# Kernel tuning notes

Measured on AMD Instinct MI355X. Metric: run time of the kernel, lower is better.

Reference implementation:

```python
import jax, jax.numpy as jnp
import numpy as np

U, I, D, B, E = 100000, 50000, 128, 4, 500000


def setup_inputs() -> dict:
    key = jax.random.key(0)
    ks = jax.random.split(key, 8)
    return {
        "init_user_embedding": jax.random.normal(ks[0], (U, D), dtype=jnp.float32),
        "init_item_embedding": jax.random.normal(ks[1], (I, D), dtype=jnp.float32),
        "edge_u": jax.random.randint(ks[2], (B, E), 0, U, dtype=jnp.int32),
        "edge_i": jax.random.randint(ks[3], (B, E), 0, I, dtype=jnp.int32),
        "edge_w": jax.random.uniform(ks[4], (B, E), dtype=jnp.float32),
        "u_w": jax.random.normal(ks[5], (D, D), dtype=jnp.float32) * (6.0 / (D + D)) ** 0.5,
        "i_w": jax.random.normal(ks[6], (D, D), dtype=jnp.float32) * (6.0 / (D + D)) ** 0.5,
        "alpha": jnp.full((1,), 0.25, dtype=jnp.float32),  # PReLU weight (default init 0.25)
    }


def reference(init_user_embedding, init_item_embedding, edge_u, edge_i, edge_w, u_w, i_w, alpha):
    # spmm per behavior: behavior_mats[b] @ item_emb and behavior_mats_t[b] @ user_emb
    def spmm_u(w, iu, ii):  # [U, D] = A[b] @ item_emb
        return jax.ops.segment_sum(w[:, None] * init_item_embedding[ii], iu, num_segments=U)

    def spmm_i(w, iu, ii):  # [I, D] = A[b].T @ user_emb
        return jax.ops.segment_sum(w[:, None] * init_user_embedding[iu], ii, num_segments=I)

    user_embs = jax.vmap(spmm_u)(edge_w, edge_u, edge_i)  # [B, U, D]
    item_embs = jax.vmap(spmm_i)(edge_w, edge_u, edge_i)  # [B, I, D]

    prelu = lambda x: jnp.where(x >= 0, x, alpha * x)

    multi_u = prelu(jnp.mean(user_embs, axis=0) @ u_w)    # [U, D]
    multi_i = prelu(jnp.mean(item_embs, axis=0) @ i_w)    # [I, D]
    single_u = prelu(jnp.einsum("bud,do->buo", user_embs, u_w))  # [B, U, D]
    single_i = prelu(jnp.einsum("bid,do->bio", item_embs, i_w))  # [B, I, D]
    return multi_u, multi_i, single_u, single_i
```

## Files before the change

### kernel.cpp

```cpp
#include <hip/hip_runtime.h>

#define U_N 100000
#define I_N 50000
#define D_N 128
#define B_N 4
#define E_N 500000
#define NEDGE (B_N * E_N)
#define NKEYU (4 * U_N)
#define NKEYS (NKEYU + 4 * I_N)
#define NMEMB (2 * NEDGE)
#define SCHUNK 2048
#define SNBLK ((NKEYS + SCHUNK - 1) / SCHUNK)
#define TBI ((I_N + 31) / 32)
#define TBU ((U_N + 31) / 32)
#define NZ4 ((NKEYS + 4) / 4)
#define ZB  ((NZ4 + 255) / 256)

typedef float f32x2 __attribute__((ext_vector_type(2)));

__device__ inline unsigned int pack_bf16(float a, float b) {
    unsigned int ua = __float_as_uint(a);
    ua += 0x7FFFu + ((ua >> 16) & 1u);
    unsigned int ub = __float_as_uint(b);
    ub += 0x7FFFu + ((ub >> 16) & 1u);
    return (ua >> 16) | (ub & 0xFFFF0000u);
}

__global__ __launch_bounds__(256) void transform2_kernel(
    const float* __restrict__ item_emb, const float* __restrict__ user_emb,
    const float* __restrict__ u_w, const float* __restrict__ i_w,
    unsigned int* __restrict__ tA, unsigned int* __restrict__ tB,
    int4* __restrict__ offs4)
{
    __shared__ float wlds[D_N][D_N];

    const float* X; const float* W; unsigned int* Y; int N; int blk;
    if (blockIdx.x < TBI) {
        X = item_emb; W = u_w; Y = tA; N = I_N; blk = blockIdx.x;
    } else if (blockIdx.x < TBI + TBU) {
        X = user_emb; W = i_w; Y = tB; N = U_N; blk = blockIdx.x - TBI;
    } else {
        int t = (blockIdx.x - TBI - TBU) * 256 + threadIdx.x;
        if (t < NZ4) offs4[t] = make_int4(0, 0, 0, 0);
        return;
    }

    for (int idx = threadIdx.x; idx < D_N * D_N / 4; idx += 256)
        reinterpret_cast<float4*>(&wlds[0][0])[idx] =
            reinterpret_cast<const float4*>(W)[idx];
    __syncthreads();

    int rr = threadIdx.x & 31;
    int cg = threadIdx.x >> 5;
    int c0 = cg * 16;
    int r  = blk * 32 + rr;
    bool valid = (r < N);
    int rc = valid ? r : (N - 1);
    const float* xrow = X + (size_t)rc * D_N;

    float4 acc[4];
    #pragma unroll
    for (int c = 0; c < 4; ++c) acc[c] = make_float4(0.f, 0.f, 0.f, 0.f);

    for (int k4 = 0; k4 < D_N / 4; ++k4) {
        float4 a = *reinterpret_cast<const float4*>(xrow + k4 * 4);
        #pragma unroll
        for (int kk = 0; kk < 4; ++kk) {
            float ak = (kk == 0) ? a.x : (kk == 1) ? a.y : (kk == 2) ? a.z : a.w;
            #pragma unroll
            for (int c = 0; c < 4; ++c) {
                const float4 wv = *reinterpret_cast<const float4*>(
                    &wlds[k4 * 4 + kk][c0 + c * 4]);
                acc[c].x += ak * wv.x;
                acc[c].y += ak * wv.y;
                acc[c].z += ak * wv.z;
                acc[c].w += ak * wv.w;
            }
        }
    }
    if (valid) {
        unsigned int* yrow = Y + (size_t)r * (D_N / 2) + c0 / 2;
        #pragma unroll
        for (int c = 0; c < 4; ++c) {
            yrow[2 * c]     = pack_bf16(acc[c].x, acc[c].y);
            yrow[2 * c + 1] = pack_bf16(acc[c].z, acc[c].w);
        }
    }
}

__global__ __launch_bounds__(256) void count_kernel(
    const int* __restrict__ eu, const int* __restrict__ ei,
    int* __restrict__ offs, int* __restrict__ rank_u, int* __restrict__ rank_i)
{
    int t = blockIdx.x * 256 + threadIdx.x;
    if (t >= NMEMB) return;
    if (t < NEDGE) {
        int e = t;
        int key = eu[e] * 4 + e / E_N;
        rank_u[e] = atomicAdd(&offs[key], 1);
    } else {
        int e = t - NEDGE;
        int key = NKEYU + ei[e] * 4 + e / E_N;
        rank_i[e] = atomicAdd(&offs[key], 1);
    }
}

__global__ __launch_bounds__(256) void scan1_kernel(
    int* __restrict__ offs, int* __restrict__ bsum)
{
    __shared__ int s[256];
    int base = blockIdx.x * SCHUNK + threadIdx.x * 8;
    int v[8]; int tsum = 0;
    #pragma unroll
    for (int j = 0; j < 8; ++j) {
        int idx = base + j;
        v[j] = (idx < NKEYS) ? offs[idx] : 0;
        tsum += v[j];
    }
    s[threadIdx.x] = tsum; __syncthreads();
    for (int off = 1; off < 256; off <<= 1) {
        int t = (threadIdx.x >= off) ? s[threadIdx.x - off] : 0;
        __syncthreads(); s[threadIdx.x] += t; __syncthreads();
    }
    int excl = s[threadIdx.x] - tsum;
    if (threadIdx.x == 255) bsum[blockIdx.x] = s[255];
    int run = excl;
    #pragma unroll
    for (int j = 0; j < 8; ++j) {
        int idx = base + j;
        if (idx < NKEYS) offs[idx] = run;
        run += v[j];
    }
}

__global__ __launch_bounds__(512) void scan2_kernel(int* __restrict__ bsum,
                                                    int* __restrict__ offs)
{
    __shared__ int s[512];
    int v = (threadIdx.x < SNBLK) ? bsum[threadIdx.x] : 0;
    s[threadIdx.x] = v; __syncthreads();
    for (int off = 1; off < 512; off <<= 1) {
        int t = (threadIdx.x >= off) ? s[threadIdx.x - off] : 0;
        __syncthreads(); s[threadIdx.x] += t; __syncthreads();
    }
    if (threadIdx.x < SNBLK) bsum[threadIdx.x] = s[threadIdx.x] - v;
    if (threadIdx.x == 511) offs[NKEYS] = s[511];
}

__global__ __launch_bounds__(256) void scan3_kernel(int* __restrict__ offs,
                                                    const int* __restrict__ bsum)
{
    int add = bsum[blockIdx.x];
    int base = blockIdx.x * SCHUNK + threadIdx.x * 8;
    #pragma unroll
    for (int j = 0; j < 8; ++j) {
        int idx = base + j;
        if (idx < NKEYS) offs[idx] += add;
    }
}

__global__ __launch_bounds__(256) void fill_kernel(
    const int* __restrict__ eu, const int* __restrict__ ei,
    const float* __restrict__ ew,
    const int* __restrict__ offs,
    const int* __restrict__ rank_u, const int* __restrict__ rank_i,
    int2* __restrict__ pairs)
{
    int t = blockIdx.x * 256 + threadIdx.x;
    if (t >= NMEMB) return;
    if (t < NEDGE) {
        int e = t;
        int b = e / E_N;
        int key = eu[e] * 4 + b;
        int pos = offs[key] + rank_u[e];
        pairs[pos] = make_int2(ei[e], __float_as_int(ew[e]));
    } else {
        int e = t - NEDGE;
        int b = e / E_N;
        int key = NKEYU + ei[e] * 4 + b;
        int pos = offs[key] + rank_i[e];
        pairs[pos] = make_int2(eu[e], __float_as_int(ew[e]));
    }
}

__global__ __launch_bounds__(256) void gather_kernel(
    const unsigned int* __restrict__ tA, const unsigned int* __restrict__ tB,
    const int2* __restrict__ pairs, const int* __restrict__ offs,
    float* __restrict__ single_u, float* __restrict__ multi_u,
    float* __restrict__ single_i, float* __restrict__ multi_i,
    const float* __restrict__ alpha_p)
{
    int rg = blockIdx.x * 4 + (threadIdx.x >> 6);
    if (rg >= U_N + I_N) return;
    bool uside = rg < U_N;
    int r = uside ? rg : rg - U_N;
    const unsigned int* T = uside ? tA : tB;
    float* single  = uside ? single_u : single_i;
    float* multi   = uside ? multi_u : multi_i;
    int N  = uside ? U_N : I_N;
    int k0 = uside ? r * 4 : NKEYU + r * 4;

    float alpha = alpha_p[0];
    int lane = threadIdx.x & 63;

    int o0 = __builtin_amdgcn_readfirstlane(offs[k0]);
    int o1 = __builtin_amdgcn_readfirstlane(offs[k0 + 1]);
    int o2 = __builtin_amdgcn_readfirstlane(offs[k0 + 2]);
    int o3 = __builtin_amdgcn_readfirstlane(offs[k0 + 3]);
    int o4 = __builtin_amdgcn_readfirstlane(offs[k0 + 4]);
    int p0 = o0, p1 = o1, p2 = o2, p3 = o3;

    float ax0 = 0.f, ay0 = 0.f, ax1 = 0.f, ay1 = 0.f;
    float ax2 = 0.f, ay2 = 0.f, ax3 = 0.f, ay3 = 0.f;

    while ((p0 < o1) | (p1 < o2) | (p2 < o3) | (p3 < o4)) {
        int a0 = p0 < o1, a1 = p1 < o2, a2 = p2 < o3, a3 = p3 < o4;
        int i0 = a0 ? p0 : o0;
        int i1 = a1 ? p1 : o0;
        int i2 = a2 ? p2 : o0;
        int i3 = a3 ? p3 : o0;
        int2 q0 = pairs[i0];
        int2 q1 = pairs[i1];
        int2 q2 = pairs[i2];
        int2 q3 = pairs[i3];
        int sx0 = __builtin_amdgcn_readfirstlane(q0.x);
        int sw0 = __builtin_amdgcn_readfirstlane(q0.y);
        int sx1 = __builtin_amdgcn_readfirstlane(q1.x);
        int sw1 = __builtin_amdgcn_readfirstlane(q1.y);
        int sx2 = __builtin_amdgcn_readfirstlane(q2.x);
        int sw2 = __builtin_amdgcn_readfirstlane(q2.y);
        int sx3 = __builtin_amdgcn_readfirstlane(q3.x);
        int sw3 = __builtin_amdgcn_readfirstlane(q3.y);
        unsigned int d0 = T[(size_t)sx0 * (D_N / 2) + lane];
        unsigned int d1 = T[(size_t)sx1 * (D_N / 2) + lane];
        unsigned int d2 = T[(size_t)sx2 * (D_N / 2) + lane];
        unsigned int d3 = T[(size_t)sx3 * (D_N / 2) + lane];
        float w0 = a0 ? __int_as_float(sw0) : 0.f;
        float w1 = a1 ? __int_as_float(sw1) : 0.f;
        float w2 = a2 ? __int_as_float(sw2) : 0.f;
        float w3 = a3 ? __int_as_float(sw3) : 0.f;
        ax0 += w0 * __uint_as_float(d0 << 16);
        ay0 += w0 * __uint_as_float(d0 & 0xFFFF0000u);
        ax1 += w1 * __uint_as_float(d1 << 16);
        ay1 += w1 * __uint_as_float(d1 & 0xFFFF0000u);
        ax2 += w2 * __uint_as_float(d2 << 16);
        ay2 += w2 * __uint_as_float(d2 & 0xFFFF0000u);
        ax3 += w3 * __uint_as_float(d3 << 16);
        ay3 += w3 * __uint_as_float(d3 & 0xFFFF0000u);
        p0 += a0; p1 += a1; p2 += a2; p3 += a3;
    }

    float mx = 0.25f * (ax0 + ax1 + ax2 + ax3);
    float my = 0.25f * (ay0 + ay1 + ay2 + ay3);

    f32x2 o;
    o.x = ax0 >= 0.f ? ax0 : alpha * ax0;
    o.y = ay0 >= 0.f ? ay0 : alpha * ay0;
    __builtin_nontemporal_store(o, reinterpret_cast<f32x2*>(
        single + ((size_t)0 * N + r) * D_N + lane * 2));
    o.x = ax1 >= 0.f ? ax1 : alpha * ax1;
    o.y = ay1 >= 0.f ? ay1 : alpha * ay1;
    __builtin_nontemporal_store(o, reinterpret_cast<f32x2*>(
        single + ((size_t)1 * N + r) * D_N + lane * 2));
    o.x = ax2 >= 0.f ? ax2 : alpha * ax2;
    o.y = ay2 >= 0.f ? ay2 : alpha * ay2;
    __builtin_nontemporal_store(o, reinterpret_cast<f32x2*>(
        single + ((size_t)2 * N + r) * D_N + lane * 2));
    o.x = ax3 >= 0.f ? ax3 : alpha * ax3;
    o.y = ay3 >= 0.f ? ay3 : alpha * ay3;
    __builtin_nontemporal_store(o, reinterpret_cast<f32x2*>(
        single + ((size_t)3 * N + r) * D_N + lane * 2));

    o.x = mx >= 0.f ? mx : alpha * mx;
    o.y = my >= 0.f ? my : alpha * my;
    __builtin_nontemporal_store(o, reinterpret_cast<f32x2*>(
        multi + (size_t)r * D_N + lane * 2));
}

extern "C" void kernel_launch(void* const* d_in, const int* in_sizes, int n_in,
                              void* d_out, int out_size, void* d_ws, size_t ws_size,
                              hipStream_t stream) {
    const float* user_emb = (const float*)d_in[0];
    const float* item_emb = (const float*)d_in[1];
    const int*   eu       = (const int*)d_in[2];
    const int*   ei       = (const int*)d_in[3];
    const float* ew       = (const float*)d_in[4];
    const float* u_w      = (const float*)d_in[5];
    const float* i_w      = (const float*)d_in[6];
    const float* alpha    = (const float*)d_in[7];

    float* out      = (float*)d_out;
    float* multi_u  = out;
    float* multi_i  = out + (size_t)U_N * D_N;
    float* single_u = out + (size_t)(U_N + I_N) * D_N;
    float* single_i = single_u + (size_t)B_N * U_N * D_N;

    int* rank_u = (int*)multi_i;
    int* rank_i = rank_u + NEDGE;

    int*  offs  = (int*)d_ws;
    int*  bsum  = offs + (NKEYS + 4);
    int2* pairs = (int2*)((char*)d_ws + ((((NKEYS + 4 + 512) * 4) + 255) & ~255));
    unsigned int* tA = (unsigned int*)(pairs + NMEMB);
    unsigned int* tB = tA + (size_t)I_N * (D_N / 2);

    transform2_kernel<<<TBI + TBU + ZB, 256, 0, stream>>>(
        item_emb, user_emb, u_w, i_w, tA, tB, (int4*)offs);
    count_kernel<<<(NMEMB + 255) / 256, 256, 0, stream>>>(eu, ei, offs,
                                                          rank_u, rank_i);
    scan1_kernel<<<SNBLK, 256, 0, stream>>>(offs, bsum);
    scan2_kernel<<<1, 512, 0, stream>>>(bsum, offs);
    scan3_kernel<<<SNBLK, 256, 0, stream>>>(offs, bsum);
    fill_kernel<<<(NMEMB + 255) / 256, 256, 0, stream>>>(eu, ei, ew, offs,
                                                         rank_u, rank_i, pairs);

    gather_kernel<<<(U_N + I_N + 3) / 4, 256, 0, stream>>>(
        tA, tB, pairs, offs,
        single_u, multi_u, single_i, multi_i, alpha);
}
```

Before: 553.9 us.

## Fuse edge counting into transform kernel and gather two edges per iteration

Splits zeroing of the offset array into its own small kernel, then merges the dense transform and the atomic edge-count pass into one launch so the two independent workloads can overlap. The transform drops its LDS staging of the weight matrix and reads weights straight from global/cache. The gather loop now loads two (index, weight) pairs at once with a 16-byte load and processes two edges per behavior per iteration, with a zeroed sentinel pair appended so the over-read stays in bounds. Removing LDS weights may raise cache traffic in the matmul, and the paired loads can be misaligned when the segment start offset is odd.

Measured after the change: 752.1 us. 35.8% more time.

```diff
diff --git a/kernel.cpp b/kernel.cpp
--- a/kernel.cpp
+++ b/kernel.cpp
@@ -13,8 +13,8 @@
 #define SNBLK ((NKEYS + SCHUNK - 1) / SCHUNK)
 #define TBI ((I_N + 31) / 32)
 #define TBU ((U_N + 31) / 32)
+#define CB  ((NMEMB + 255) / 256)
 #define NZ4 ((NKEYS + 4) / 4)
-#define ZB  ((NZ4 + 255) / 256)
 
 typedef float f32x2 __attribute__((ext_vector_type(2)));
 
@@ -26,29 +26,42 @@
     return (ua >> 16) | (ub & 0xFFFF0000u);
 }
 
-__global__ __launch_bounds__(256) void transform2_kernel(
+__global__ __launch_bounds__(256) void zero_kernel(int4* __restrict__ offs4,
+                                                   int2* __restrict__ sentinel)
+{
+    int t = blockIdx.x * 256 + threadIdx.x;
+    if (t < NZ4) offs4[t] = make_int4(0, 0, 0, 0);
+    if (t == 0) { sentinel[0] = make_int2(0, 0); sentinel[1] = make_int2(0, 0); }
+}
+
+__global__ __launch_bounds__(256) void work_kernel(
     const float* __restrict__ item_emb, const float* __restrict__ user_emb,
     const float* __restrict__ u_w, const float* __restrict__ i_w,
     unsigned int* __restrict__ tA, unsigned int* __restrict__ tB,
-    int4* __restrict__ offs4)
-{
-    __shared__ float wlds[D_N][D_N];
+    const int* __restrict__ eu, const int* __restrict__ ei,
+    int* __restrict__ offs, int* __restrict__ rank_u, int* __restrict__ rank_i)
+{
+    if (blockIdx.x >= TBI + TBU) {
+        int t = (blockIdx.x - TBI - TBU) * 256 + threadIdx.x;
+        if (t >= NMEMB) return;
+        if (t < NEDGE) {
+            int e = t;
+            int key = eu[e] * 4 + e / E_N;
+            rank_u[e] = atomicAdd(&offs[key], 1);
+        } else {
+            int e = t - NEDGE;
+            int key = NKEYU + ei[e] * 4 + e / E_N;
+            rank_i[e] = atomicAdd(&offs[key], 1);
+        }
+        return;
+    }
 
     const float* X; const float* W; unsigned int* Y; int N; int blk;
     if (blockIdx.x < TBI) {
         X = item_emb; W = u_w; Y = tA; N = I_N; blk = blockIdx.x;
-    } else if (blockIdx.x < TBI + TBU) {
+    } else {
         X = user_emb; W = i_w; Y = tB; N = U_N; blk = blockIdx.x - TBI;
-    } else {
-        int t = (blockIdx.x - TBI - TBU) * 256 + threadIdx.x;
-        if (t < NZ4) offs4[t] = make_int4(0, 0, 0, 0);
-        return;
-    }
-
-    for (int idx = threadIdx.x; idx < D_N * D_N / 4; idx += 256)
-        reinterpret_cast<float4*>(&wlds[0][0])[idx] =
-            reinterpret_cast<const float4*>(W)[idx];
-    __syncthreads();
+    }
 
     int rr = threadIdx.x & 31;
     int cg = threadIdx.x >> 5;
@@ -67,10 +80,10 @@
         #pragma unroll
         for (int kk = 0; kk < 4; ++kk) {
             float ak = (kk == 0) ? a.x : (kk == 1) ? a.y : (kk == 2) ? a.z : a.w;
+            const float* wrow = W + (size_t)(k4 * 4 + kk) * D_N + c0;
             #pragma unroll
             for (int c = 0; c < 4; ++c) {
-                const float4 wv = *reinterpret_cast<const float4*>(
-                    &wlds[k4 * 4 + kk][c0 + c * 4]);
+                const float4 wv = *reinterpret_cast<const float4*>(wrow + c * 4);
                 acc[c].x += ak * wv.x;
                 acc[c].y += ak * wv.y;
                 acc[c].z += ak * wv.z;
@@ -85,23 +98,6 @@
             yrow[2 * c]     = pack_bf16(acc[c].x, acc[c].y);
             yrow[2 * c + 1] = pack_bf16(acc[c].z, acc[c].w);
         }
-    }
-}
-
-__global__ __launch_bounds__(256) void count_kernel(
-    const int* __restrict__ eu, const int* __restrict__ ei,
-    int* __restrict__ offs, int* __restrict__ rank_u, int* __restrict__ rank_i)
-{
-    int t = blockIdx.x * 256 + threadIdx.x;
-    if (t >= NMEMB) return;
-    if (t < NEDGE) {
-        int e = t;
-        int key = eu[e] * 4 + e / E_N;
-        rank_u[e] = atomicAdd(&offs[key], 1);
-    } else {
-        int e = t - NEDGE;
-        int key = NKEYU + ei[e] * 4 + e / E_N;
-        rank_i[e] = atomicAdd(&offs[key], 1);
     }
 }
 
@@ -214,40 +210,67 @@
     float ax2 = 0.f, ay2 = 0.f, ax3 = 0.f, ay3 = 0.f;
 
     while ((p0 < o1) | (p1 < o2) | (p2 < o3) | (p3 < o4)) {
-        int a0 = p0 < o1, a1 = p1 < o2, a2 = p2 < o3, a3 = p3 < o4;
+        int a0 = p0 < o1, b0 = (p0 + 1) < o1;
+        int a1 = p1 < o2, b1 = (p1 + 1) < o2;
+        int a2 = p2 < o3, b2 = (p2 + 1) < o3;
+        int a3 = p3 < o4, b3 = (p3 + 1) < o4;
         int i0 = a0 ? p0 : o0;
         int i1 = a1 ? p1 : o0;
         int i2 = a2 ? p2 : o0;
         int i3 = a3 ? p3 : o0;
-        int2 q0 = pairs[i0];
-        int2 q1 = pairs[i1];
-        int2 q2 = pairs[i2];
-        int2 q3 = pairs[i3];
-        int sx0 = __builtin_amdgcn_readfirstlane(q0.x);
-        int sw0 = __builtin_amdgcn_readfirstlane(q0.y);
-        int sx1 = __builtin_amdgcn_readfirstlane(q1.x);
-        int sw1 = __builtin_amdgcn_readfirstlane(q1.y);
-        int sx2 = __builtin_amdgcn_readfirstlane(q2.x);
-        int sw2 = __builtin_amdgcn_readfirstlane(q2.y);
-        int sx3 = __builtin_amdgcn_readfirstlane(q3.x);
-        int sw3 = __builtin_amdgcn_readfirstlane(q3.y);
-        unsigned int d0 = T[(size_t)sx0 * (D_N / 2) + lane];
-        unsigned int d1 = T[(size_t)sx1 * (D_N / 2) + lane];
-        unsigned int d2 = T[(size_t)sx2 * (D_N / 2) + lane];
-        unsigned int d3 = T[(size_t)sx3 * (D_N / 2) + lane];
-        float w0 = a0 ? __int_as_float(sw0) : 0.f;
-        float w1 = a1 ? __int_as_float(sw1) : 0.f;
-        float w2 = a2 ? __int_as_float(sw2) : 0.f;
-        float w3 = a3 ? __int_as_float(sw3) : 0.f;
-        ax0 += w0 * __uint_as_float(d0 << 16);
-        ay0 += w0 * __uint_as_float(d0 & 0xFFFF0000u);
-        ax1 += w1 * __uint_as_float(d1 << 16);
-        ay1 += w1 * __uint_as_float(d1 & 0xFFFF0000u);
-        ax2 += w2 * __uint_as_float(d2 << 16);
-        ay2 += w2 * __uint_as_float(d2 & 0xFFFF0000u);
-        ax3 += w3 * __uint_as_float(d3 << 16);
-        ay3 += w3 * __uint_as_float(d3 & 0xFFFF0000u);
-        p0 += a0; p1 += a1; p2 += a2; p3 += a3;
+        int4 Q0 = *reinterpret_cast<const int4*>(pairs + i0);
+        int4 Q1 = *reinterpret_cast<const int4*>(pairs + i1);
+        int4 Q2 = *reinterpret_cast<const int4*>(pairs + i2);
+        int4 Q3 = *reinterpret_cast<const int4*>(pairs + i3);
+        int sx0a = __builtin_amdgcn_readfirstlane(Q0.x);
+        int sw0a = __builtin_amdgcn_readfirstlane(Q0.y);
+        int sx0b = __builtin_amdgcn_readfirstlane(Q0.z);
+        int sw0b = __builtin_amdgcn_readfirstlane(Q0.w);
+        int sx1a = __builtin_amdgcn_readfirstlane(Q1.x);
+        int sw1a = __builtin_amdgcn_readfirstlane(Q1.y);
+        int sx1b = __builtin_amdgcn_readfirstlane(Q1.z);
+        int sw1b = __builtin_amdgcn_readfirstlane(Q1.w);
+        int sx2a = __builtin_amdgcn_readfirstlane(Q2.x);
+        int sw2a = __builtin_amdgcn_readfirstlane(Q2.y);
+        int sx2b = __builtin_amdgcn_readfirstlane(Q2.z);
+        int sw2b = __builtin_amdgcn_readfirstlane(Q2.w);
+        int sx3a = __builtin_amdgcn_readfirstlane(Q3.x);
+        int sw3a = __builtin_amdgcn_readfirstlane(Q3.y);
+        int sx3b = __builtin_amdgcn_readfirstlane(Q3.z);
+        int sw3b = __builtin_amdgcn_readfirstlane(Q3.w);
+        unsigned int d0a = T[(size_t)sx0a * (D_N / 2) + lane];
+        unsigned int d0b = T[(size_t)sx0b * (D_N / 2) + lane];
+        unsigned int d1a = T[(size_t)sx1a * (D_N / 2) + lane];
+        unsigned int d1b = T[(size_t)sx1b * (D_N / 2) + lane];
+        unsigned int d2a = T[(size_t)sx2a * (D_N / 2) + lane];
+        unsigned int d2b = T[(size_t)sx2b * (D_N / 2) + lane];
+        unsigned int d3a = T[(size_t)sx3a * (D_N / 2) + lane];
+        unsigned int d3b = T[(size_t)sx3b * (D_N / 2) + lane];
+        float w0a = a0 ? __int_as_float(sw0a) : 0.f;
+        float w0b = b0 ? __int_as_float(sw0b) : 0.f;
+        float w1a = a1 ? __int_as_float(sw1a) : 0.f;
+        float w1b = b1 ? __int_as_float(sw1b) : 0.f;
+        float w2a = a2 ? __int_as_float(sw2a) : 0.f;
+        float w2b = b2 ? __int_as_float(sw2b) : 0.f;
+        float w3a = a3 ? __int_as_float(sw3a) : 0.f;
+        float w3b = b3 ? __int_as_float(sw3b) : 0.f;
+        ax0 += w0a * __uint_as_float(d0a << 16)
+             + w0b * __uint_as_float(d0b << 16);
+        ay0 += w0a * __uint_as_float(d0a & 0xFFFF0000u)
+             + w0b * __uint_as_float(d0b & 0xFFFF0000u);
+        ax1 += w1a * __uint_as_float(d1a << 16)
+             + w1b * __uint_as_float(d1b << 16);
+        ay1 += w1a * __uint_as_float(d1a & 0xFFFF0000u)
+             + w1b * __uint_as_float(d1b & 0xFFFF0000u);
+        ax2 += w2a * __uint_as_float(d2a << 16)
+             + w2b * __uint_as_float(d2b << 16);
+        ay2 += w2a * __uint_as_float(d2a & 0xFFFF0000u)
+             + w2b * __uint_as_float(d2b & 0xFFFF0000u);
+        ax3 += w3a * __uint_as_float(d3a << 16)
+             + w3b * __uint_as_float(d3b << 16);
+        ay3 += w3a * __uint_as_float(d3a & 0xFFFF0000u)
+             + w3b * __uint_as_float(d3b & 0xFFFF0000u);
+        p0 += a0 + b0; p1 += a1 + b1; p2 += a2 + b2; p3 += a3 + b3;
     }
 
     float mx = 0.25f * (ax0 + ax1 + ax2 + ax3);
@@ -301,19 +324,18 @@
     int*  offs  = (int*)d_ws;
     int*  bsum  = offs + (NKEYS + 4);
     int2* pairs = (int2*)((char*)d_ws + ((((NKEYS + 4 + 512) * 4) + 255) & ~255));
-    unsigned int* tA = (unsigned int*)(pairs + NMEMB);
+    unsigned int* tA = (unsigned int*)(pairs + NMEMB + 2);
     unsigned int* tB = tA + (size_t)I_N * (D_N / 2);
 
-    transform2_kernel<<<TBI + TBU + ZB, 256, 0, stream>>>(
-        item_emb, user_emb, u_w, i_w, tA, tB, (int4*)offs);
-    count_kernel<<<(NMEMB + 255) / 256, 256, 0, stream>>>(eu, ei, offs,
-                                                          rank_u, rank_i);
+    zero_kernel<<<(NZ4 + 255) / 256, 256, 0, stream>>>((int4*)offs,
+                                                       pairs + NMEMB);
+    work_kernel<<<TBI + TBU + CB, 256, 0, stream>>>(
+        item_emb, user_emb, u_w, i_w, tA, tB, eu, ei, offs, rank_u, rank_i);
     scan1_kernel<<<SNBLK, 256, 0, stream>>>(offs, bsum);
     scan2_kernel<<<1, 512, 0, stream>>>(bsum, offs);
     scan3_kernel<<<SNBLK, 256, 0, stream>>>(offs, bsum);
-    fill_kernel<<<(NMEMB + 255) / 256, 256, 0, stream>>>(eu, ei, ew, offs,
-                                                         rank_u, rank_i, pairs);
-
+    fill_kernel<<<CB, 256, 0, stream>>>(eu, ei, ew, offs,
+                                        rank_u, rank_i, pairs);
     gather_kernel<<<(U_N + I_N + 3) / 4, 256, 0, stream>>>(
         tA, tB, pairs, offs,
         single_u, multi_u, single_i, multi_i, alpha);
```
